# Optimization experiments

Hardware: AMD Instinct MI355X
Metric: run time of the kernel (lower is better)

## Reference

```python
import jax, jax.numpy as jnp
import numpy as np

EPS = 1e-3


def setup_inputs() -> dict:
    key = jax.random.key(0)
    k1, k2 = jax.random.split(key)
    U, N, C_in, C_out = 40000, 32, 9, 64
    inputs = jax.random.normal(k1, (U, N, C_in), dtype=jnp.float32)
    # torch nn.Linear weight has shape (out, in)
    W = jax.random.normal(k2, (C_out, C_in), dtype=jnp.float32) * (1.0 / np.sqrt(C_in))
    gamma = jnp.ones((C_out,), dtype=jnp.float32)
    beta = jnp.zeros((C_out,), dtype=jnp.float32)
    return {"inputs": inputs, "W": W, "gamma": gamma, "beta": beta}


def reference(inputs, W, gamma, beta):
    # Linear (no bias): (U, N, C_in) x (C_out, C_in) -> (U, N, C_out)
    x = jnp.einsum('unc,oc->uno', inputs, W)
    # BatchNorm1d in training mode: stats over batch and points dims (U, N),
    # biased variance, as torch uses for normalization.
    mean = jnp.mean(x, axis=(0, 1))            # (C_out,)
    var = jnp.var(x, axis=(0, 1))              # (C_out,) biased
    x = (x - mean) * jax.lax.rsqrt(var + EPS) * gamma + beta
    x = jax.nn.relu(x)
    # Max over points dim, keepdim -> (U, 1, C_out)
    return jnp.max(x, axis=1, keepdims=True)
```

## Files before the change

kernel.cpp:

```cpp
#include <hip/hip_runtime.h>
#include <math.h>

#define U_TOTAL 40000
#define N_PTS   32
#define C_IN    9
#define C_OUT   64
#define UPW     4
#define UPB     (UPW * 4)
#define NBLK_A  (U_TOTAL / UPB)
#define EPSV    1e-3f

typedef float  f32x2  __attribute__((ext_vector_type(2)));
typedef float  f32x16 __attribute__((ext_vector_type(16)));
typedef short  short8 __attribute__((ext_vector_type(8)));
typedef float  f32x4u __attribute__((ext_vector_type(4), aligned(4)));

__device__ __forceinline__ unsigned pk_bf16(float lo, float hi) {
    unsigned r;
    asm("v_cvt_pk_bf16_f32 %0, %1, %2" : "=v"(r) : "v"(lo), "v"(hi));
    return r;
}

__global__ __launch_bounds__(256, 6)
void pfn_a(const float* __restrict__ in, const float* __restrict__ Wg,
           float* __restrict__ out, float* __restrict__ partials)
{
    __shared__ float red[4][2][64];

    const int tid  = threadIdx.x;
    const int lane = tid & 63;
    const int w    = tid >> 6;
    const int col  = lane & 31;
    const int g    = lane >> 5;

    const float* wr0 = Wg + (size_t)col * C_IN + g * 4;
    const float* wr1 = Wg + (size_t)(32 + col) * C_IN + g * 4;
    float a0 = wr0[0], a1 = wr0[1], a2 = wr0[2], a3 = wr0[3];
    float c0 = wr1[0], c1 = wr1[1], c2 = wr1[2], c3 = wr1[3];
    float k8a = g ? 0.f : Wg[(size_t)col * C_IN + 8];
    float k8c = g ? 0.f : Wg[(size_t)(32 + col) * C_IN + 8];
    union { unsigned u[4]; short8 v; } B0, B1;
    B0.u[0] = pk_bf16(a0, a1);  B0.u[1] = pk_bf16(a2, a3);
    B0.u[2] = pk_bf16(k8a, 0.f); B0.u[3] = 0u;
    B1.u[0] = pk_bf16(c0, c1);  B1.u[1] = pk_bf16(c2, c3);
    B1.u[2] = pk_bf16(k8c, 0.f); B1.u[3] = 0u;

    const int u0 = blockIdx.x * UPB + w * UPW;
    const float* base = in + (size_t)u0 * (N_PTS * C_IN) + col * C_IN;
    f32x4u q[UPW];
    float  f8[UPW];
#pragma unroll
    for (int t = 0; t < UPW; ++t) {
        const float* rp = base + t * (N_PTS * C_IN);
        q[t]  = *(const f32x4u*)(rp + 4 * g);
        f8[t] = rp[8];
    }

    f32x2 S1_0 = {0.f,0.f}, S2_0 = {0.f,0.f}, S1_1 = {0.f,0.f}, S2_1 = {0.f,0.f};

#pragma unroll
    for (int t = 0; t < UPW; ++t) {
        union { unsigned u[4]; short8 v; } A;
        A.u[0] = pk_bf16(q[t].x, q[t].y);
        A.u[1] = pk_bf16(q[t].z, q[t].w);
        A.u[2] = pk_bf16(g ? 0.f : f8[t], 0.f);
        A.u[3] = 0u;

        f32x16 z = {};
        f32x16 d0 = __builtin_amdgcn_mfma_f32_32x32x16_bf16(A.v, B0.v, z, 0, 0, 0);
        f32x16 d1 = __builtin_amdgcn_mfma_f32_32x32x16_bf16(A.v, B1.v, z, 0, 0, 0);

        union { f32x16 v; f32x2 p[8]; } D0, D1;
        D0.v = d0; D1.v = d1;
        f32x2 mx0 = D0.p[0], mx1 = D1.p[0];
#pragma unroll
        for (int i = 0; i < 8; ++i) {
            S1_0 += D0.p[i];
            S2_0 = __builtin_elementwise_fma(D0.p[i], D0.p[i], S2_0);
            S1_1 += D1.p[i];
            S2_1 = __builtin_elementwise_fma(D1.p[i], D1.p[i], S2_1);
            if (i) {
                mx0 = __builtin_elementwise_max(mx0, D0.p[i]);
                mx1 = __builtin_elementwise_max(mx1, D1.p[i]);
            }
        }
        float m0 = fmaxf(mx0.x, mx0.y);
        float m1 = fmaxf(mx1.x, mx1.y);
        m0 = fmaxf(m0, __shfl_xor(m0, 32));
        m1 = fmaxf(m1, __shfl_xor(m1, 32));
        out[(size_t)(u0 + t) * C_OUT + lane] = g ? m1 : m0;
    }

    float s1_0 = S1_0.x + S1_0.y, s2_0 = S2_0.x + S2_0.y;
    float s1_1 = S1_1.x + S1_1.y, s2_1 = S2_1.x + S2_1.y;
    s1_0 += __shfl_xor(s1_0, 32);
    s2_0 += __shfl_xor(s2_0, 32);
    s1_1 += __shfl_xor(s1_1, 32);
    s2_1 += __shfl_xor(s2_1, 32);
    if (g == 0) {
        red[w][0][col]      = s1_0;
        red[w][0][32 + col] = s1_1;
        red[w][1][col]      = s2_0;
        red[w][1][32 + col] = s2_1;
    }
    __syncthreads();
    if (tid < 128) {
        const int o = tid >> 1, k = tid & 1;
        float acc = red[0][k][o] + red[1][k][o] + red[2][k][o] + red[3][k][o];
        partials[(size_t)blockIdx.x * 128 + tid] = acc;
    }
}

__global__ __launch_bounds__(256)
void pfn_reduce(const float* __restrict__ partials, float* __restrict__ sums, int nblocks)
{
    const int b = blockIdx.x;
    const int t = threadIdx.x;
    float acc = 0.f;
    for (int i = t; i < nblocks; i += 256) acc += partials[(size_t)i * 128 + b];
    __shared__ float r[256];
    r[t] = acc;
    __syncthreads();
    for (int s = 128; s > 0; s >>= 1) {
        if (t < s) r[t] += r[t + s];
        __syncthreads();
    }
    if (t == 0) sums[b] = r[0];
}

__global__ __launch_bounds__(256)
void pfn_c(float* __restrict__ out, const float* __restrict__ sums,
           const float* __restrict__ gamma, const float* __restrict__ beta)
{
    const int idx = blockIdx.x * 256 + threadIdx.x;
    const int o = (idx & 15) * 4;
    const float invM = 1.0f / (float)(U_TOTAL * N_PTS);
    float4 v   = ((const float4*)out)[idx];
    float4 s01 = ((const float4*)sums)[(2 * o) / 4];
    float4 s23 = ((const float4*)sums)[(2 * o) / 4 + 1];
    float4 g4  = ((const float4*)gamma)[o / 4];
    float4 b4  = ((const float4*)beta)[o / 4];

#define BN1(x, S1, S2, g, b) ({                                   \
        float mean_ = (S1) * invM;                                \
        float var_  = (S2) * invM - mean_ * mean_;                \
        float sc_   = (g) * __frsqrt_rn(var_ + EPSV);             \
        fmaxf(fmaf((x), sc_, (b) - mean_ * sc_), 0.0f); })

    v.x = BN1(v.x, s01.x, s01.y, g4.x, b4.x);
    v.y = BN1(v.y, s01.z, s01.w, g4.y, b4.y);
    v.z = BN1(v.z, s23.x, s23.y, g4.z, b4.z);
    v.w = BN1(v.w, s23.z, s23.w, g4.w, b4.w);
#undef BN1
    ((float4*)out)[idx] = v;
}

extern "C" void kernel_launch(void* const* d_in, const int* in_sizes, int n_in,
                              void* d_out, int out_size, void* d_ws, size_t ws_size,
                              hipStream_t stream)
{
    const float* in    = (const float*)d_in[0];
    const float* Wg    = (const float*)d_in[1];
    const float* gamma = (const float*)d_in[2];
    const float* beta  = (const float*)d_in[3];
    float* out = (float*)d_out;

    float* partials = (float*)d_ws;
    float* sums     = partials + (size_t)NBLK_A * 128;

    pfn_a<<<NBLK_A, 256, 0, stream>>>(in, Wg, out, partials);
    pfn_reduce<<<128, 256, 0, stream>>>(partials, sums, NBLK_A);
    pfn_c<<<(U_TOTAL * C_OUT / 4) / 256, 256, 0, stream>>>(out, sums, gamma, beta);
}
```

Baseline: 27.54 us.

## Transpose partials layout for coalesced reduce and serialize MFMA epilogues

Block partials are now stored channel-major, so the reduce kernel reads a contiguous row per channel instead of striding by 128 floats, which makes its loads coalesced. The two MFMA results are now computed and reduced one after the other in separate scopes to cut live accumulator registers, and the occupancy hint drops from 6 to 5. In exchange, the writes in the first kernel become scattered stores, and serializing the two MFMAs may reduce overlap between matrix and vector work.

After: 27.53 us. About the same (-0.0%).

```diff
diff --git a/kernel.cpp b/kernel.cpp
--- a/kernel.cpp
+++ b/kernel.cpp
@@ -21,7 +21,7 @@
     return r;
 }
 
-__global__ __launch_bounds__(256, 6)
+__global__ __launch_bounds__(256, 5)
 void pfn_a(const float* __restrict__ in, const float* __restrict__ Wg,
            float* __restrict__ out, float* __restrict__ partials)
 {
@@ -67,27 +67,33 @@
         A.u[3] = 0u;
 
         f32x16 z = {};
-        f32x16 d0 = __builtin_amdgcn_mfma_f32_32x32x16_bf16(A.v, B0.v, z, 0, 0, 0);
-        f32x16 d1 = __builtin_amdgcn_mfma_f32_32x32x16_bf16(A.v, B1.v, z, 0, 0, 0);
-
-        union { f32x16 v; f32x2 p[8]; } D0, D1;
-        D0.v = d0; D1.v = d1;
-        f32x2 mx0 = D0.p[0], mx1 = D1.p[0];
+        float m0, m1;
+        {
+            f32x16 d0 = __builtin_amdgcn_mfma_f32_32x32x16_bf16(A.v, B0.v, z, 0, 0, 0);
+            union { f32x16 v; f32x2 p[8]; } D; D.v = d0;
+            f32x2 mx = D.p[0];
 #pragma unroll
-        for (int i = 0; i < 8; ++i) {
-            S1_0 += D0.p[i];
-            S2_0 = __builtin_elementwise_fma(D0.p[i], D0.p[i], S2_0);
-            S1_1 += D1.p[i];
-            S2_1 = __builtin_elementwise_fma(D1.p[i], D1.p[i], S2_1);
-            if (i) {
-                mx0 = __builtin_elementwise_max(mx0, D0.p[i]);
-                mx1 = __builtin_elementwise_max(mx1, D1.p[i]);
+            for (int i = 0; i < 8; ++i) {
+                S1_0 += D.p[i];
+                S2_0 = __builtin_elementwise_fma(D.p[i], D.p[i], S2_0);
+                if (i) mx = __builtin_elementwise_max(mx, D.p[i]);
             }
+            m0 = fmaxf(mx.x, mx.y);
+            m0 = fmaxf(m0, __shfl_xor(m0, 32));
         }
-        float m0 = fmaxf(mx0.x, mx0.y);
-        float m1 = fmaxf(mx1.x, mx1.y);
-        m0 = fmaxf(m0, __shfl_xor(m0, 32));
-        m1 = fmaxf(m1, __shfl_xor(m1, 32));
+        {
+            f32x16 d1 = __builtin_amdgcn_mfma_f32_32x32x16_bf16(A.v, B1.v, z, 0, 0, 0);
+            union { f32x16 v; f32x2 p[8]; } D; D.v = d1;
+            f32x2 mx = D.p[0];
+#pragma unroll
+            for (int i = 0; i < 8; ++i) {
+                S1_1 += D.p[i];
+                S2_1 = __builtin_elementwise_fma(D.p[i], D.p[i], S2_1);
+                if (i) mx = __builtin_elementwise_max(mx, D.p[i]);
+            }
+            m1 = fmaxf(mx.x, mx.y);
+            m1 = fmaxf(m1, __shfl_xor(m1, 32));
+        }
         out[(size_t)(u0 + t) * C_OUT + lane] = g ? m1 : m0;
     }
 
@@ -107,7 +113,7 @@
     if (tid < 128) {
         const int o = tid >> 1, k = tid & 1;
         float acc = red[0][k][o] + red[1][k][o] + red[2][k][o] + red[3][k][o];
-        partials[(size_t)blockIdx.x * 128 + tid] = acc;
+        partials[(size_t)tid * NBLK_A + blockIdx.x] = acc;
     }
 }
 
@@ -116,8 +122,9 @@
 {
     const int b = blockIdx.x;
     const int t = threadIdx.x;
+    const float* row = partials + (size_t)b * nblocks;
     float acc = 0.f;
-    for (int i = t; i < nblocks; i += 256) acc += partials[(size_t)i * 128 + b];
+    for (int i = t; i < nblocks; i += 256) acc += row[i];
     __shared__ float r[256];
     r[t] = acc;
     __syncthreads();
@@ -166,7 +173,7 @@
     float* out = (float*)d_out;
 
     float* partials = (float*)d_ws;
-    float* sums     = partials + (size_t)NBLK_A * 128;
+    float* sums     = partials + (size_t)128 * NBLK_A;
 
     pfn_a<<<NBLK_A, 256, 0, stream>>>(in, Wg, out, partials);
     pfn_reduce<<<128, 256, 0, stream>>>(partials, sums, NBLK_A);
```

## Use persistent grid with double-buffered tile loads and transposed partials layout

Applied to the files above, without the earlier changes.

The first kernel now launches a fixed grid of 1024 blocks. Each block processes two or three 16-unit tiles, and the next tile's global loads are issued before the current tile is computed, so memory latency overlaps with MFMA work. Because there are far fewer blocks, the partial-sum array shrinks, and it is stored channel-major so the reduce kernel reads contiguously. The MFMA epilogues are split to reduce register pressure, and the occupancy hint drops from 6 to 4, trading occupancy for more in-flight loads per wave.

Result: slower. 50.45 us (+83.2%).

```diff
diff --git a/kernel.cpp b/kernel.cpp
--- a/kernel.cpp
+++ b/kernel.cpp
@@ -6,8 +6,9 @@
 #define C_IN    9
 #define C_OUT   64
 #define UPW     4
-#define UPB     (UPW * 4)
-#define NBLK_A  (U_TOTAL / UPB)
+#define UPB     16
+#define TILES   (U_TOTAL / UPB)
+#define GRID_A  1024
 #define EPSV    1e-3f
 
 typedef float  f32x2  __attribute__((ext_vector_type(2)));
@@ -21,7 +22,19 @@
     return r;
 }
 
-__global__ __launch_bounds__(256, 6)
+__device__ __forceinline__ void issue_tile(const float* __restrict__ in, int tile,
+                                           int w, int col, int g,
+                                           f32x4u (&q)[UPW], float (&f8)[UPW]) {
+    const float* base = in + (size_t)(tile * UPB + w * UPW) * (N_PTS * C_IN) + col * C_IN;
+#pragma unroll
+    for (int t = 0; t < UPW; ++t) {
+        const float* rp = base + t * (N_PTS * C_IN);
+        q[t]  = *(const f32x4u*)(rp + 4 * g);
+        f8[t] = rp[8];
+    }
+}
+
+__global__ __launch_bounds__(256, 4)
 void pfn_a(const float* __restrict__ in, const float* __restrict__ Wg,
            float* __restrict__ out, float* __restrict__ partials)
 {
@@ -32,6 +45,7 @@
     const int w    = tid >> 6;
     const int col  = lane & 31;
     const int g    = lane >> 5;
+    const int bid  = blockIdx.x;
 
     const float* wr0 = Wg + (size_t)col * C_IN + g * 4;
     const float* wr1 = Wg + (size_t)(32 + col) * C_IN + g * 4;
@@ -45,51 +59,61 @@
     B1.u[0] = pk_bf16(c0, c1);  B1.u[1] = pk_bf16(c2, c3);
     B1.u[2] = pk_bf16(k8c, 0.f); B1.u[3] = 0u;
 
-    const int u0 = blockIdx.x * UPB + w * UPW;
-    const float* base = in + (size_t)u0 * (N_PTS * C_IN) + col * C_IN;
-    f32x4u q[UPW];
-    float  f8[UPW];
-#pragma unroll
-    for (int t = 0; t < UPW; ++t) {
-        const float* rp = base + t * (N_PTS * C_IN);
-        q[t]  = *(const f32x4u*)(rp + 4 * g);
-        f8[t] = rp[8];
-    }
-
     f32x2 S1_0 = {0.f,0.f}, S2_0 = {0.f,0.f}, S1_1 = {0.f,0.f}, S2_1 = {0.f,0.f};
 
-#pragma unroll
-    for (int t = 0; t < UPW; ++t) {
-        union { unsigned u[4]; short8 v; } A;
-        A.u[0] = pk_bf16(q[t].x, q[t].y);
-        A.u[1] = pk_bf16(q[t].z, q[t].w);
-        A.u[2] = pk_bf16(g ? 0.f : f8[t], 0.f);
-        A.u[3] = 0u;
+#define COMPUTE_STORE_TILE(TILE, Q, F8)                                        \
+    do {                                                                       \
+        const int u0_ = (TILE) * UPB + w * UPW;                                \
+        _Pragma("unroll")                                                      \
+        for (int t = 0; t < UPW; ++t) {                                        \
+            union { unsigned u[4]; short8 v; } A;                              \
+            A.u[0] = pk_bf16(Q[t].x, Q[t].y);                                  \
+            A.u[1] = pk_bf16(Q[t].z, Q[t].w);                                  \
+            A.u[2] = pk_bf16(g ? 0.f : F8[t], 0.f);                            \
+            A.u[3] = 0u;                                                       \
+            const f32x16 z_ = {};                                              \
+            float m0_, m1_;                                                    \
+            {                                                                  \
+                f32x16 d_ = __builtin_amdgcn_mfma_f32_32x32x16_bf16(A.v, B0.v, z_, 0, 0, 0); \
+                union { f32x16 v; f32x2 p[8]; } D_; D_.v = d_;                 \
+                f32x2 mx_ = D_.p[0];                                           \
+                _Pragma("unroll")                                              \
+                for (int i = 0; i < 8; ++i) {                                  \
+                    S1_0 += D_.p[i];                                           \
+                    S2_0 = __builtin_elementwise_fma(D_.p[i], D_.p[i], S2_0);  \
+                    if (i) mx_ = __builtin_elementwise_max(mx_, D_.p[i]);      \
+                }                                                              \
+                m0_ = fmaxf(mx_.x, mx_.y);                                     \
+                m0_ = fmaxf(m0_, __shfl_xor(m0_, 32));                         \
+            }                                                                  \
+            {                                                                  \
+                f32x16 d_ = __builtin_amdgcn_mfma_f32_32x32x16_bf16(A.v, B1.v, z_, 0, 0, 0); \
+                union { f32x16 v; f32x2 p[8]; } D_; D_.v = d_;                 \
+                f32x2 mx_ = D_.p[0];                                           \
+                _Pragma("unroll")                                              \
+                for (int i = 0; i < 8; ++i) {                                  \
+                    S1_1 += D_.p[i];                                           \
+                    S2_1 = __builtin_elementwise_fma(D_.p[i], D_.p[i], S2_1);  \
+                    if (i) mx_ = __builtin_elementwise_max(mx_, D_.p[i]);      \
+                }                                                              \
+                m1_ = fmaxf(mx_.x, mx_.y);                                     \
+                m1_ = fmaxf(m1_, __shfl_xor(m1_, 32));                         \
+            }                                                                  \
+            out[(size_t)(u0_ + t) * C_OUT + lane] = g ? m1_ : m0_;             \
+        }                                                                      \
+    } while (0)
 
-        f32x16 z = {};
-        f32x16 d0 = __builtin_amdgcn_mfma_f32_32x32x16_bf16(A.v, B0.v, z, 0, 0, 0);
-        f32x16 d1 = __builtin_amdgcn_mfma_f32_32x32x16_bf16(A.v, B1.v, z, 0, 0, 0);
+    const bool has2 = (bid + 2 * GRID_A) < TILES;
+    f32x4u qA[UPW], qB[UPW];
+    float  f8A[UPW], f8B[UPW];
 
-        union { f32x16 v; f32x2 p[8]; } D0, D1;
-        D0.v = d0; D1.v = d1;
-        f32x2 mx0 = D0.p[0], mx1 = D1.p[0];
-#pragma unroll
-        for (int i = 0; i < 8; ++i) {
-            S1_0 += D0.p[i];
-            S2_0 = __builtin_elementwise_fma(D0.p[i], D0.p[i], S2_0);
-            S1_1 += D1.p[i];
-            S2_1 = __builtin_elementwise_fma(D1.p[i], D1.p[i], S2_1);
-            if (i) {
-                mx0 = __builtin_elementwise_max(mx0, D0.p[i]);
-                mx1 = __builtin_elementwise_max(mx1, D1.p[i]);
-            }
-        }
-        float m0 = fmaxf(mx0.x, mx0.y);
-        float m1 = fmaxf(mx1.x, mx1.y);
-        m0 = fmaxf(m0, __shfl_xor(m0, 32));
-        m1 = fmaxf(m1, __shfl_xor(m1, 32));
-        out[(size_t)(u0 + t) * C_OUT + lane] = g ? m1 : m0;
-    }
+    issue_tile(in, bid,          w, col, g, qA, f8A);
+    issue_tile(in, bid + GRID_A, w, col, g, qB, f8B);
+    COMPUTE_STORE_TILE(bid, qA, f8A);
+    if (has2) issue_tile(in, bid + 2 * GRID_A, w, col, g, qA, f8A);
+    COMPUTE_STORE_TILE(bid + GRID_A, qB, f8B);
+    if (has2) COMPUTE_STORE_TILE(bid + 2 * GRID_A, qA, f8A);
+#undef COMPUTE_STORE_TILE
 
     float s1_0 = S1_0.x + S1_0.y, s2_0 = S2_0.x + S2_0.y;
     float s1_1 = S1_1.x + S1_1.y, s2_1 = S2_1.x + S2_1.y;
@@ -107,7 +131,7 @@
     if (tid < 128) {
         const int o = tid >> 1, k = tid & 1;
         float acc = red[0][k][o] + red[1][k][o] + red[2][k][o] + red[3][k][o];
-        partials[(size_t)blockIdx.x * 128 + tid] = acc;
+        partials[(size_t)tid * GRID_A + bid] = acc;
     }
 }
 
@@ -116,8 +140,9 @@
 {
     const int b = blockIdx.x;
     const int t = threadIdx.x;
+    const float* row = partials + (size_t)b * nblocks;
     float acc = 0.f;
-    for (int i = t; i < nblocks; i += 256) acc += partials[(size_t)i * 128 + b];
+    for (int i = t; i < nblocks; i += 256) acc += row[i];
     __shared__ float r[256];
     r[t] = acc;
     __syncthreads();
@@ -166,9 +191,9 @@
     float* out = (float*)d_out;
 
     float* partials = (float*)d_ws;
-    float* sums     = partials + (size_t)NBLK_A * 128;
+    float* sums     = partials + (size_t)128 * GRID_A;
 
-    pfn_a<<<NBLK_A, 256, 0, stream>>>(in, Wg, out, partials);
-    pfn_reduce<<<128, 256, 0, stream>>>(partials, sums, NBLK_A);
+    pfn_a<<<GRID_A, 256, 0, stream>>>(in, Wg, out, partials);
+    pfn_reduce<<<128, 256, 0, stream>>>(partials, sums, GRID_A);
     pfn_c<<<(U_TOTAL * C_OUT / 4) / 256, 256, 0, stream>>>(out, sums, gamma, beta);
 }
```
